# Kernel optimization log

Hardware: AMD Instinct MI355X
Metric: run time of the kernel (lower is better)

The kernel has to match this reference:

```python
import jax, jax.numpy as jnp
import numpy as np

N_NODES = 100000
NINP = 128
N_EDGES = 1600000
EPS = 1e-12


def _gcn_conv(x, W, b, src, dst, deg_inv_sqrt):
    # PyG GCNConv: h = x W; out = D^{-1/2}(A+I)D^{-1/2} h + b
    h = x @ W  # [N, out_dim]
    norm = deg_inv_sqrt[src] * deg_inv_sqrt[dst]  # [E]
    agg = jax.ops.segment_sum(h[src] * norm[:, None], dst, num_segments=N_NODES)
    # self-loop contribution: weight deg_inv_sqrt[i]^2
    agg = agg + h * (deg_inv_sqrt ** 2)[:, None]
    return agg + b


def setup_inputs() -> dict:
    key = jax.random.key(0)
    k1, k2, k3, k4 = jax.random.split(key, 4)
    edge_index = jax.random.randint(k1, (2, N_EDGES), 0, N_NODES, dtype=jnp.int64)
    # embedding table (xavier-normal-like), padding_idx=0 row zeroed
    emb = jax.random.normal(k2, (N_NODES, NINP), dtype=jnp.float32) * (2.0 / (N_NODES + NINP)) ** 0.5
    emb = emb.at[0].set(0.0)
    W1 = jax.random.normal(k3, (NINP, 2 * NINP), dtype=jnp.float32) * (1.0 / NINP) ** 0.5
    b1 = jnp.zeros((2 * NINP,), dtype=jnp.float32)
    W2 = jax.random.normal(k4, (2 * NINP, NINP), dtype=jnp.float32) * (1.0 / (2 * NINP)) ** 0.5
    b2 = jnp.zeros((NINP,), dtype=jnp.float32)
    return {"emb": emb, "W1": W1, "b1": b1, "W2": W2, "b2": b2, "edge_index": edge_index}


def reference(emb, W1, b1, W2, b2, edge_index):
    src, dst = edge_index[0], edge_index[1]
    # symmetric GCN degree with self-loops (in-degree on dst + 1)
    deg = jax.ops.segment_sum(jnp.ones_like(dst, dtype=emb.dtype), dst, num_segments=N_NODES) + 1.0
    deg_inv_sqrt = jax.lax.rsqrt(deg)
    x = _gcn_conv(emb, W1, b1, src, dst, deg_inv_sqrt)  # [N, 2*ninp]
    # F.normalize(p=2, dim=-1)
    x = x / jnp.maximum(jnp.linalg.norm(x, axis=-1, keepdims=True), EPS)
    # dropout in eval mode (identity)
    out = _gcn_conv(x, W2, b2, src, dst, deg_inv_sqrt)  # [N, ninp]
    return out
```

## Files before the change

kernel.cpp:

```cpp
#include <hip/hip_runtime.h>
#include <hip/hip_bf16.h>

typedef __attribute__((ext_vector_type(8))) short bf16x8;
typedef __attribute__((ext_vector_type(4))) float f32x4;

#define NBUCK 391
#define BCAP 8192


__device__ __forceinline__ ushort f2bf(float f) {
    unsigned int b = __float_as_uint(f);
    unsigned int r = (b + 0x7fffu + ((b >> 16) & 1u)) >> 16;
    return (ushort)r;
}
__device__ __forceinline__ float bflo(uint v) { return __uint_as_float(v << 16); }
__device__ __forceinline__ float bfhi(uint v) { return __uint_as_float(v & 0xffff0000u); }


__global__ __launch_bounds__(256) void prep_kernel(const float* __restrict__ W1, ushort* __restrict__ W1t,
                                                   const float* __restrict__ W2, ushort* __restrict__ W2t,
                                                   int* __restrict__ gcur) {
    int b = blockIdx.x, t = threadIdx.x;
    if (b == 0) {
        if (t < NBUCK) gcur[t] = 0;
        if (t + 256 < NBUCK) gcur[t + 256] = 0;
    } else if (b <= 128) {
        int i = (b - 1) * 256 + t;
        int n = i >> 7, k = i & 127;
        W1t[i] = f2bf(W1[(size_t)k * 256 + n]);
    } else {
        int i = (b - 129) * 256 + t;
        int n = i >> 8, k = i & 255;
        W2t[i] = f2bf(W2[(size_t)k * 128 + n]);
    }
}


__global__ __launch_bounds__(256) void bucket_kernel(const int* __restrict__ src, const int* __restrict__ dst,
                                                     int* __restrict__ gcur, int2* __restrict__ pairs,
                                                     int E, int chunk) {
    __shared__ int lcnt[NBUCK];
    for (int t = threadIdx.x; t < NBUCK; t += 256) lcnt[t] = 0;
    __syncthreads();
    int e0 = blockIdx.x * chunk;
    int e1 = e0 + chunk; if (e1 > E) e1 = E;
    for (int e = e0 + (int)threadIdx.x; e < e1; e += 256)
        atomicAdd(&lcnt[dst[e] >> 8], 1);
    __syncthreads();
    for (int t = threadIdx.x; t < NBUCK; t += 256) {
        int c = lcnt[t];
        lcnt[t] = c ? atomicAdd(&gcur[t], c) : 0;
    }
    __syncthreads();
    for (int e = e0 + (int)threadIdx.x; e < e1; e += 256) {
        int d = dst[e], s = src[e];
        int b = d >> 8;
        int p = atomicAdd(&lcnt[b], 1);
        if (p < BCAP) pairs[(size_t)b * BCAP + p] = make_int2(d, s);
    }
}


__global__ __launch_bounds__(512) void scan_buckets(const int* __restrict__ gcur, int* __restrict__ bbase,
                                                    int* __restrict__ offs, int Nn, int E) {
    int i = threadIdx.x;
    int v = (i < NBUCK) ? min(gcur[i], BCAP) : 0;
    int lane = i & 63, wid = i >> 6;
    int x = v;
#pragma unroll
    for (int d = 1; d < 64; d <<= 1) {
        int y = __shfl_up(x, d, 64);
        if (lane >= d) x += y;
    }
    __shared__ int wsum[8], wpre[8];
    if (lane == 63) wsum[wid] = x;
    __syncthreads();
    if (i == 0) {
        int run = 0;
        for (int w = 0; w < 8; ++w) { wpre[w] = run; run += wsum[w]; }
        offs[Nn] = E;
    }
    __syncthreads();
    if (i < NBUCK) bbase[i] = x - v + wpre[wid];
}


__global__ __launch_bounds__(256) void csr_kernel(const int2* __restrict__ pairs, const int* __restrict__ gcur,
                                                  const int* __restrict__ bbase,
                                                  int* __restrict__ offs, float* __restrict__ dis,
                                                  int* __restrict__ csr, int Nn) {
    int b = blockIdx.x;
    int n0 = b << 8;
    int ne = min(gcur[b], BCAP);
    __shared__ int cnt[256], off[256], pos[256];
    int i = threadIdx.x;
    cnt[i] = 0;
    __syncthreads();
    const int2* pp = pairs + (size_t)b * BCAP;
    for (int e = i; e < ne; e += 256)
        atomicAdd(&cnt[pp[e].x - n0], 1);
    __syncthreads();
    int lane = i & 63, wid = i >> 6;
    int v = cnt[i];
    int x = v;
#pragma unroll
    for (int d = 1; d < 64; d <<= 1) {
        int y = __shfl_up(x, d, 64);
        if (lane >= d) x += y;
    }
    __shared__ int wsum[4], wpre[4];
    if (lane == 63) wsum[wid] = x;
    __syncthreads();
    if (i == 0) {
        int run = 0;
        for (int w = 0; w < 4; ++w) { wpre[w] = run; run += wsum[w]; }
    }
    __syncthreads();
    int excl = x - v + wpre[wid];
    off[i] = excl;
    pos[i] = 0;
    int n = n0 + i;
    if (n < Nn) {
        offs[n] = bbase[b] + excl;
        dis[n] = rsqrtf((float)v + 1.0f);
    }
    __syncthreads();
    int base = bbase[b];
    for (int e = i; e < ne; e += 256) {
        int2 r = pp[e];
        int li = r.x - n0;
        int p = atomicAdd(&pos[li], 1);
        csr[base + off[li] + p] = r.y;
    }
}


__global__ void cast_scale_kernel(const float4* __restrict__ in, const float* __restrict__ dis,
                                  ushort4* __restrict__ out, int n4) {
    int stride = gridDim.x * blockDim.x;
    for (int i = blockIdx.x * blockDim.x + threadIdx.x; i < n4; i += stride) {
        float s = dis[i >> 5];
        float4 v = in[i];
        ushort4 o;
        o.x = f2bf(v.x * s); o.y = f2bf(v.y * s); o.z = f2bf(v.z * s); o.w = f2bf(v.w * s);
        out[i] = o;
    }
}


template <bool BIAS, bool BF16OUT>
__global__ __launch_bounds__(256) void agg_kernel(const uint* __restrict__ tbl,
                                                  const int* __restrict__ offs,
                                                  const int* __restrict__ rec,
                                                  const float* __restrict__ dis,
                                                  const float* __restrict__ bias,
                                                  void* __restrict__ outp, int Nn) {
    int gw = (int)((blockIdx.x * 256 + threadIdx.x) >> 6);
    uint lane = threadIdx.x & 63;
    if (gw >= Nn) return;
    float dn = dis[gw];
    int e0 = offs[gw], e1 = offs[gw + 1];
    uint hv = tbl[(uint)gw * 64u + lane];
    float ax = bflo(hv), ay = bfhi(hv);

    for (int base = e0; base < e1; base += 16) {
        int ee = base + (int)(lane & 15u);
        uint rr = (uint)rec[ee < e1 ? ee : e1 - 1];
        uint vv[16];
#pragma unroll
        for (int j = 0; j < 16; ++j) {
            uint idx = (uint)__shfl((int)rr, j, 64);
            vv[j] = tbl[idx * 64u + lane];
        }
#pragma unroll
        for (int j = 0; j < 16; ++j) {
            uint v = (base + j < e1) ? vv[j] : 0u;
            ax += bflo(v);
            ay += bfhi(v);
        }
    }

    ax *= dn; ay *= dn;
    if (BIAS) {
        float2 bv = reinterpret_cast<const float2*>(bias)[lane];
        ax += bv.x; ay += bv.y;
    }
    if (BF16OUT) {
        reinterpret_cast<uint*>(outp)[(uint)gw * 64u + lane] =
            (uint)f2bf(ax) | ((uint)f2bf(ay) << 16);
    } else {
        float2 o; o.x = ax; o.y = ay;
        reinterpret_cast<float2*>(outp)[(uint)gw * 64u + lane] = o;
    }
}


__global__ __launch_bounds__(256, 2) void fused_gemm(const ushort* __restrict__ A,
                                                     const ushort* __restrict__ W1t,
                                                     const float* __restrict__ bias1,
                                                     const ushort* __restrict__ W2t,
                                                     const float* __restrict__ dsc,
                                                     ushort* __restrict__ out2, int M) {
    __shared__ ushort xt[64 * 256];
    __shared__ float ssl[4][64];
    int lane = threadIdx.x & 63, wid = threadIdx.x >> 6;
    int m0 = blockIdx.x * 64;
    int koff = (lane >> 4) * 8;

    bf16x8 a[4][4], b1f[4][4];
#pragma unroll
    for (int ms = 0; ms < 4; ++ms) {
        int r = m0 + ms * 16 + (lane & 15);
        if (r >= M) r = M - 1;
        const bf16x8* p = reinterpret_cast<const bf16x8*>(A + (size_t)r * 128 + koff);
#pragma unroll
        for (int ks = 0; ks < 4; ++ks) a[ms][ks] = p[ks * 4];
    }
#pragma unroll
    for (int ns = 0; ns < 4; ++ns) {
        int c = wid * 64 + ns * 16 + (lane & 15);
        const bf16x8* p = reinterpret_cast<const bf16x8*>(W1t + (size_t)c * 128 + koff);
#pragma unroll
        for (int ks = 0; ks < 4; ++ks) b1f[ns][ks] = p[ks * 4];
    }

    f32x4 acc[4][4];
#pragma unroll
    for (int ms = 0; ms < 4; ++ms)
#pragma unroll
        for (int ns = 0; ns < 4; ++ns) acc[ms][ns] = (f32x4){0.f, 0.f, 0.f, 0.f};
#pragma unroll
    for (int ks = 0; ks < 4; ++ks)
#pragma unroll
        for (int ms = 0; ms < 4; ++ms)
#pragma unroll
            for (int ns = 0; ns < 4; ++ns)
                acc[ms][ns] = __builtin_amdgcn_mfma_f32_16x16x32_bf16(a[ms][ks], b1f[ns][ks], acc[ms][ns], 0, 0, 0);

    bf16x8 b2f[2][8];
#pragma unroll
    for (int ns = 0; ns < 2; ++ns) {
        int c = wid * 32 + ns * 16 + (lane & 15);
        const bf16x8* p = reinterpret_cast<const bf16x8*>(W2t + (size_t)c * 256 + koff);
#pragma unroll
        for (int ks = 0; ks < 8; ++ks) b2f[ns][ks] = p[ks * 4];
    }

    float bv[4];
#pragma unroll
    for (int ns = 0; ns < 4; ++ns) bv[ns] = bias1[wid * 64 + ns * 16 + (lane & 15)];
    float ps[4][4];
#pragma unroll
    for (int ms = 0; ms < 4; ++ms)
#pragma unroll
        for (int r = 0; r < 4; ++r) {
            float s = 0.f;
#pragma unroll
            for (int ns = 0; ns < 4; ++ns) {
                float v = acc[ms][ns][r] + bv[ns];
                acc[ms][ns][r] = v;
                s += v * v;
            }
            ps[ms][r] = s;
        }
#pragma unroll
    for (int d = 1; d < 16; d <<= 1)
#pragma unroll
        for (int ms = 0; ms < 4; ++ms)
#pragma unroll
            for (int r = 0; r < 4; ++r) ps[ms][r] += __shfl_xor(ps[ms][r], d, 64);
    if ((lane & 15) == 0) {
#pragma unroll
        for (int ms = 0; ms < 4; ++ms)
#pragma unroll
            for (int r = 0; r < 4; ++r) ssl[wid][ms * 16 + (lane >> 4) * 4 + r] = ps[ms][r];
    }
    __syncthreads();
#pragma unroll
    for (int ms = 0; ms < 4; ++ms)
#pragma unroll
        for (int r = 0; r < 4; ++r) {
            int rt = ms * 16 + (lane >> 4) * 4 + r;
            float tot = ssl[0][rt] + ssl[1][rt] + ssl[2][rt] + ssl[3][rt];
            float inv = 1.0f / fmaxf(sqrtf(tot), 1e-12f);
            int sw = (rt & 7) << 3;
#pragma unroll
            for (int ns = 0; ns < 4; ++ns) {
                int col = wid * 64 + ns * 16 + (lane & 15);
                xt[(rt * 256 + col) ^ sw] = f2bf(acc[ms][ns][r] * inv);
            }
        }
    __syncthreads();

    f32x4 acc2[4][2];
#pragma unroll
    for (int ms = 0; ms < 4; ++ms)
#pragma unroll
        for (int ns = 0; ns < 2; ++ns) acc2[ms][ns] = (f32x4){0.f, 0.f, 0.f, 0.f};
#pragma unroll
    for (int ks = 0; ks < 8; ++ks) {
        bf16x8 a2[4];
#pragma unroll
        for (int ms = 0; ms < 4; ++ms) {
            int rowA = ms * 16 + (lane & 15);
            int eb = (rowA * 256 + koff + ks * 32) ^ ((rowA & 7) << 3);
            a2[ms] = *reinterpret_cast<const bf16x8*>(&xt[eb]);
        }
#pragma unroll
        for (int ms = 0; ms < 4; ++ms)
#pragma unroll
            for (int ns = 0; ns < 2; ++ns)
                acc2[ms][ns] = __builtin_amdgcn_mfma_f32_16x16x32_bf16(a2[ms], b2f[ns][ks], acc2[ms][ns], 0, 0, 0);
    }
#pragma unroll
    for (int ms = 0; ms < 4; ++ms)
#pragma unroll
        for (int r = 0; r < 4; ++r) {
            int row = m0 + ms * 16 + (lane >> 4) * 4 + r;
            if (row < M) {
                float sc = dsc[row];
#pragma unroll
                for (int ns = 0; ns < 2; ++ns)
                    out2[(size_t)row * 128 + wid * 32 + ns * 16 + (lane & 15)] =
                        f2bf(acc2[ms][ns][r] * sc);
            }
        }
}


extern "C" void kernel_launch(void* const* d_in, const int* in_sizes, int n_in,
                              void* d_out, int out_size, void* d_ws, size_t ws_size,
                              hipStream_t stream) {
    const float* emb = (const float*)d_in[0];
    const float* W1 = (const float*)d_in[1];
    const float* b1 = (const float*)d_in[2];
    const float* W2 = (const float*)d_in[3];
    const float* b2 = (const float*)d_in[4];
    const int* eidx = (const int*)d_in[5];

    const int Nn = in_sizes[0] / 128;
    const int E = in_sizes[5] / 2;
    const int* srcp = eidx;
    const int* dstp = eidx + E;

    float* ws = (float*)d_ws;
    size_t o = 0;
    uint* tbl1 = (uint*)(ws + o);  o += (size_t)Nn * 64;
    uint* axb = (uint*)(ws + o);   o += (size_t)Nn * 64;
    uint* tbl2 = (uint*)(ws + o);  o += (size_t)Nn * 64;
    ushort* W1t = (ushort*)(ws + o); o += 128 * 256 / 2;
    ushort* W2t = (ushort*)(ws + o); o += 256 * 128 / 2;
    float* dis = ws + o;    o += Nn;
    int* gcur = (int*)(ws + o);   o += NBUCK + 1;
    int* bbase = (int*)(ws + o);  o += NBUCK + 1;
    int* offs = (int*)(ws + o);   o += Nn + 16;
    int* csr = (int*)(ws + o);    o += E;
    int2* pairs = (int2*)(ws + o); o += (size_t)NBUCK * BCAP * 2;

    prep_kernel<<<257, 256, 0, stream>>>(W1, W1t, W2, W2t, gcur);

    int B1B = 512;
    int chunk = (E + B1B - 1) / B1B;
    bucket_kernel<<<B1B, 256, 0, stream>>>(srcp, dstp, gcur, pairs, E, chunk);
    scan_buckets<<<1, 512, 0, stream>>>(gcur, bbase, offs, Nn, E);
    csr_kernel<<<NBUCK, 256, 0, stream>>>(pairs, gcur, bbase, offs, dis, csr, Nn);

    int n4 = Nn * 128 / 4;
    cast_scale_kernel<<<2048, 256, 0, stream>>>((const float4*)emb, dis, (ushort4*)tbl1, n4);

    agg_kernel<false, true><<<(Nn + 3) / 4, 256, 0, stream>>>(tbl1, offs, csr, dis, nullptr, axb, Nn);
    fused_gemm<<<(Nn + 63) / 64, 256, 0, stream>>>((const ushort*)axb, W1t, b1, W2t, dis, (ushort*)tbl2, Nn);

    agg_kernel<true, false><<<(Nn + 3) / 4, 256, 0, stream>>>(tbl2, offs, csr, dis, b2, d_out, Nn);
}
```

Before: 244.2 us.

## Give each wavefront whole rows in fused GEMM to drop block-level syncs

The fused two-layer GEMM kernel is restructured so each wavefront owns 16 complete rows across all 256 hidden columns, rather than a 64-column slice of 64 rows shared by the block. The row L2-norm is then reduced with intra-wave shuffles alone, and the normalized tile goes into a per-wave LDS region, which removes both __syncthreads and the cross-wave partial-sum array. The cost is that every wave now loads the full W1 and W2 weight fragments from global/L2 inside the k-loops instead of holding a per-wave slice in registers, so weight traffic per wave rises and register pressure shifts.

New measurement: 294.2 us. 1.2x slower.

```diff
diff --git a/kernel.cpp b/kernel.cpp
--- a/kernel.cpp
+++ b/kernel.cpp
@@ -201,130 +201,93 @@
                                                      const ushort* __restrict__ W2t,
                                                      const float* __restrict__ dsc,
                                                      ushort* __restrict__ out2, int M) {
-    __shared__ ushort xt[64 * 256];
-    __shared__ float ssl[4][64];
+    __shared__ __align__(16) char xls[4 * 8192];
     int lane = threadIdx.x & 63, wid = threadIdx.x >> 6;
-    int m0 = blockIdx.x * 64;
-    int koff = (lane >> 4) * 8;
-
-    bf16x8 a[4][4], b1f[4][4];
-#pragma unroll
-    for (int ms = 0; ms < 4; ++ms) {
-        int r = m0 + ms * 16 + (lane & 15);
-        if (r >= M) r = M - 1;
-        const bf16x8* p = reinterpret_cast<const bf16x8*>(A + (size_t)r * 128 + koff);
-#pragma unroll
-        for (int ks = 0; ks < 4; ++ks) a[ms][ks] = p[ks * 4];
-    }
-#pragma unroll
-    for (int ns = 0; ns < 4; ++ns) {
-        int c = wid * 64 + ns * 16 + (lane & 15);
-        const bf16x8* p = reinterpret_cast<const bf16x8*>(W1t + (size_t)c * 128 + koff);
-#pragma unroll
-        for (int ks = 0; ks < 4; ++ks) b1f[ns][ks] = p[ks * 4];
-    }
-
-    f32x4 acc[4][4];
-#pragma unroll
-    for (int ms = 0; ms < 4; ++ms)
-#pragma unroll
-        for (int ns = 0; ns < 4; ++ns) acc[ms][ns] = (f32x4){0.f, 0.f, 0.f, 0.f};
-#pragma unroll
-    for (int ks = 0; ks < 4; ++ks)
-#pragma unroll
-        for (int ms = 0; ms < 4; ++ms)
-#pragma unroll
-            for (int ns = 0; ns < 4; ++ns)
-                acc[ms][ns] = __builtin_amdgcn_mfma_f32_16x16x32_bf16(a[ms][ks], b1f[ns][ks], acc[ms][ns], 0, 0, 0);
-
-    bf16x8 b2f[2][8];
-#pragma unroll
-    for (int ns = 0; ns < 2; ++ns) {
-        int c = wid * 32 + ns * 16 + (lane & 15);
-        const bf16x8* p = reinterpret_cast<const bf16x8*>(W2t + (size_t)c * 256 + koff);
-#pragma unroll
-        for (int ks = 0; ks < 8; ++ks) b2f[ns][ks] = p[ks * 4];
-    }
-
-    float bv[4];
-#pragma unroll
-    for (int ns = 0; ns < 4; ++ns) bv[ns] = bias1[wid * 64 + ns * 16 + (lane & 15)];
-    float ps[4][4];
-#pragma unroll
-    for (int ms = 0; ms < 4; ++ms)
-#pragma unroll
-        for (int r = 0; r < 4; ++r) {
-            float s = 0.f;
-#pragma unroll
-            for (int ns = 0; ns < 4; ++ns) {
-                float v = acc[ms][ns][r] + bv[ns];
-                acc[ms][ns][r] = v;
-                s += v * v;
-            }
-            ps[ms][r] = s;
-        }
+    int g = lane >> 4;
+    int i15 = lane & 15;
+    int koff = g * 8;
+    int r0 = blockIdx.x * 64 + wid * 16;
+    char* lds = xls + wid * 8192;
+
+    int arow = r0 + i15; if (arow >= M) arow = M - 1;
+    const bf16x8* ap = reinterpret_cast<const bf16x8*>(A + (size_t)arow * 128 + koff);
+    bf16x8 af[4];
+#pragma unroll
+    for (int ks = 0; ks < 4; ++ks) af[ks] = ap[ks * 4];
+
+    f32x4 acc[16];
+#pragma unroll
+    for (int ns = 0; ns < 16; ++ns) acc[ns] = (f32x4){0.f, 0.f, 0.f, 0.f};
+
+#pragma unroll
+    for (int ks = 0; ks < 4; ++ks) {
+        bf16x8 bf_[16];
+#pragma unroll
+        for (int ns = 0; ns < 16; ++ns)
+            bf_[ns] = *reinterpret_cast<const bf16x8*>(W1t + (size_t)(ns * 16 + i15) * 128 + ks * 32 + koff);
+#pragma unroll
+        for (int ns = 0; ns < 16; ++ns)
+            acc[ns] = __builtin_amdgcn_mfma_f32_16x16x32_bf16(af[ks], bf_[ns], acc[ns], 0, 0, 0);
+    }
+
+    float ps[4];
+#pragma unroll
+    for (int r = 0; r < 4; ++r) {
+        float s = 0.f;
+#pragma unroll
+        for (int ns = 0; ns < 16; ++ns) {
+            float v = acc[ns][r] + bias1[ns * 16 + i15];
+            acc[ns][r] = v;
+            s += v * v;
+        }
+        ps[r] = s;
+    }
 #pragma unroll
     for (int d = 1; d < 16; d <<= 1)
 #pragma unroll
-        for (int ms = 0; ms < 4; ++ms)
-#pragma unroll
-            for (int r = 0; r < 4; ++r) ps[ms][r] += __shfl_xor(ps[ms][r], d, 64);
-    if ((lane & 15) == 0) {
-#pragma unroll
-        for (int ms = 0; ms < 4; ++ms)
-#pragma unroll
-            for (int r = 0; r < 4; ++r) ssl[wid][ms * 16 + (lane >> 4) * 4 + r] = ps[ms][r];
-    }
-    __syncthreads();
-#pragma unroll
-    for (int ms = 0; ms < 4; ++ms)
-#pragma unroll
-        for (int r = 0; r < 4; ++r) {
-            int rt = ms * 16 + (lane >> 4) * 4 + r;
-            float tot = ssl[0][rt] + ssl[1][rt] + ssl[2][rt] + ssl[3][rt];
-            float inv = 1.0f / fmaxf(sqrtf(tot), 1e-12f);
-            int sw = (rt & 7) << 3;
-#pragma unroll
-            for (int ns = 0; ns < 4; ++ns) {
-                int col = wid * 64 + ns * 16 + (lane & 15);
-                xt[(rt * 256 + col) ^ sw] = f2bf(acc[ms][ns][r] * inv);
-            }
-        }
-    __syncthreads();
-
-    f32x4 acc2[4][2];
-#pragma unroll
-    for (int ms = 0; ms < 4; ++ms)
-#pragma unroll
-        for (int ns = 0; ns < 2; ++ns) acc2[ms][ns] = (f32x4){0.f, 0.f, 0.f, 0.f};
+        for (int r = 0; r < 4; ++r) ps[r] += __shfl_xor(ps[r], d, 64);
+    float inv[4];
+#pragma unroll
+    for (int r = 0; r < 4; ++r) inv[r] = 1.0f / fmaxf(sqrtf(ps[r]), 1e-12f);
+
+#pragma unroll
+    for (int r = 0; r < 4; ++r) {
+        int rt = g * 4 + r;
+        int sw = (rt & 7) << 4;
+#pragma unroll
+        for (int ns = 0; ns < 16; ++ns) {
+            int byte = rt * 512 + (ns * 16 + i15) * 2;
+            *reinterpret_cast<ushort*>(lds + (byte ^ sw)) = f2bf(acc[ns][r] * inv[r]);
+        }
+    }
+
+    f32x4 acc2[8];
+#pragma unroll
+    for (int ns = 0; ns < 8; ++ns) acc2[ns] = (f32x4){0.f, 0.f, 0.f, 0.f};
+    int sw2 = (i15 & 7) << 4;
 #pragma unroll
     for (int ks = 0; ks < 8; ++ks) {
-        bf16x8 a2[4];
-#pragma unroll
-        for (int ms = 0; ms < 4; ++ms) {
-            int rowA = ms * 16 + (lane & 15);
-            int eb = (rowA * 256 + koff + ks * 32) ^ ((rowA & 7) << 3);
-            a2[ms] = *reinterpret_cast<const bf16x8*>(&xt[eb]);
-        }
-#pragma unroll
-        for (int ms = 0; ms < 4; ++ms)
-#pragma unroll
-            for (int ns = 0; ns < 2; ++ns)
-                acc2[ms][ns] = __builtin_amdgcn_mfma_f32_16x16x32_bf16(a2[ms], b2f[ns][ks], acc2[ms][ns], 0, 0, 0);
-    }
-#pragma unroll
-    for (int ms = 0; ms < 4; ++ms)
-#pragma unroll
-        for (int r = 0; r < 4; ++r) {
-            int row = m0 + ms * 16 + (lane >> 4) * 4 + r;
-            if (row < M) {
-                float sc = dsc[row];
-#pragma unroll
-                for (int ns = 0; ns < 2; ++ns)
-                    out2[(size_t)row * 128 + wid * 32 + ns * 16 + (lane & 15)] =
-                        f2bf(acc2[ms][ns][r] * sc);
-            }
-        }
+        int rbyte = i15 * 512 + ks * 64 + g * 16;
+        bf16x8 a2 = *reinterpret_cast<const bf16x8*>(lds + (rbyte ^ sw2));
+        bf16x8 b2[8];
+#pragma unroll
+        for (int ns = 0; ns < 8; ++ns)
+            b2[ns] = *reinterpret_cast<const bf16x8*>(W2t + (size_t)(ns * 16 + i15) * 256 + ks * 32 + koff);
+#pragma unroll
+        for (int ns = 0; ns < 8; ++ns)
+            acc2[ns] = __builtin_amdgcn_mfma_f32_16x16x32_bf16(a2, b2[ns], acc2[ns], 0, 0, 0);
+    }
+
+#pragma unroll
+    for (int r = 0; r < 4; ++r) {
+        int row = r0 + g * 4 + r;
+        if (row < M) {
+            float sc = dsc[row];
+#pragma unroll
+            for (int ns = 0; ns < 8; ++ns)
+                out2[(size_t)row * 128 + ns * 16 + i15] = f2bf(acc2[ns][r] * sc);
+        }
+    }
 }
 
 
```

## Fuse first-layer aggregation into the fused GEMM kernel via shared memory

Applied to the files above, without the earlier changes.

The first-layer neighbor aggregation is moved into the fused GEMM kernel. Each wave gathers and sums bf16 neighbor rows for 16 nodes and writes the aggregated tile into swizzled shared memory, which the MFMA GEMM then reads. This removes one kernel launch and the global write and re-read of the intermediate aggregated buffer. In exchange, gather latency now runs inside a kernel limited to about 2 blocks per CU by its shared-memory and register use, so occupancy for the irregular gathers may be lower than in the standalone aggregation kernel.

After: 283.2 us. +16.0%, slower.

```diff
diff --git a/kernel.cpp b/kernel.cpp
--- a/kernel.cpp
+++ b/kernel.cpp
@@ -195,30 +195,69 @@
 }
 
 
-__global__ __launch_bounds__(256, 2) void fused_gemm(const ushort* __restrict__ A,
-                                                     const ushort* __restrict__ W1t,
-                                                     const float* __restrict__ bias1,
-                                                     const ushort* __restrict__ W2t,
-                                                     const float* __restrict__ dsc,
-                                                     ushort* __restrict__ out2, int M) {
-    __shared__ ushort xt[64 * 256];
+__global__ __launch_bounds__(256, 2) void fused_all(const uint* __restrict__ tbl,
+                                                    const int* __restrict__ offs,
+                                                    const int* __restrict__ rec,
+                                                    const float* __restrict__ dis,
+                                                    const ushort* __restrict__ W1t,
+                                                    const float* __restrict__ bias1,
+                                                    const ushort* __restrict__ W2t,
+                                                    ushort* __restrict__ out2, int M) {
+    __shared__ __align__(16) char xls[64 * 256 * 2];
     __shared__ float ssl[4][64];
     int lane = threadIdx.x & 63, wid = threadIdx.x >> 6;
+    int g = lane >> 4;
+    int i15 = lane & 15;
+    int koff = g * 8;
     int m0 = blockIdx.x * 64;
-    int koff = (lane >> 4) * 8;
+
+    for (int t = 0; t < 16; ++t) {
+        int local = wid * 16 + t;
+        int gw = m0 + local;
+        uint res = 0;
+        if (gw < M) {
+            float dn = dis[gw];
+            int e0 = offs[gw], e1 = offs[gw + 1];
+            uint hv = tbl[(uint)gw * 64u + lane];
+            float ax = bflo(hv), ay = bfhi(hv);
+            for (int base = e0; base < e1; base += 16) {
+                int ee = base + i15;
+                uint rr = (uint)rec[ee < e1 ? ee : e1 - 1];
+                uint vv[16];
+#pragma unroll
+                for (int j = 0; j < 16; ++j) {
+                    uint idx = (uint)__shfl((int)rr, j, 64);
+                    vv[j] = tbl[idx * 64u + lane];
+                }
+#pragma unroll
+                for (int j = 0; j < 16; ++j) {
+                    uint v = (base + j < e1) ? vv[j] : 0u;
+                    ax += bflo(v);
+                    ay += bfhi(v);
+                }
+            }
+            ax *= dn; ay *= dn;
+            res = (uint)f2bf(ax) | ((uint)f2bf(ay) << 16);
+        }
+        int byte = local * 256 + (int)lane * 4;
+        *reinterpret_cast<uint*>(xls + (byte ^ ((local & 7) << 4))) = res;
+    }
+    __syncthreads();
 
     bf16x8 a[4][4], b1f[4][4];
 #pragma unroll
     for (int ms = 0; ms < 4; ++ms) {
-        int r = m0 + ms * 16 + (lane & 15);
-        if (r >= M) r = M - 1;
-        const bf16x8* p = reinterpret_cast<const bf16x8*>(A + (size_t)r * 128 + koff);
-#pragma unroll
-        for (int ks = 0; ks < 4; ++ks) a[ms][ks] = p[ks * 4];
+        int row = ms * 16 + i15;
+        int sw = (row & 7) << 4;
+#pragma unroll
+        for (int ks = 0; ks < 4; ++ks) {
+            int byte = row * 256 + g * 16 + ks * 64;
+            a[ms][ks] = *reinterpret_cast<const bf16x8*>(xls + (byte ^ sw));
+        }
     }
 #pragma unroll
     for (int ns = 0; ns < 4; ++ns) {
-        int c = wid * 64 + ns * 16 + (lane & 15);
+        int c = wid * 64 + ns * 16 + i15;
         const bf16x8* p = reinterpret_cast<const bf16x8*>(W1t + (size_t)c * 128 + koff);
 #pragma unroll
         for (int ks = 0; ks < 4; ++ks) b1f[ns][ks] = p[ks * 4];
@@ -240,7 +279,7 @@
     bf16x8 b2f[2][8];
 #pragma unroll
     for (int ns = 0; ns < 2; ++ns) {
-        int c = wid * 32 + ns * 16 + (lane & 15);
+        int c = wid * 32 + ns * 16 + i15;
         const bf16x8* p = reinterpret_cast<const bf16x8*>(W2t + (size_t)c * 256 + koff);
 #pragma unroll
         for (int ks = 0; ks < 8; ++ks) b2f[ns][ks] = p[ks * 4];
@@ -248,7 +287,7 @@
 
     float bv[4];
 #pragma unroll
-    for (int ns = 0; ns < 4; ++ns) bv[ns] = bias1[wid * 64 + ns * 16 + (lane & 15)];
+    for (int ns = 0; ns < 4; ++ns) bv[ns] = bias1[wid * 64 + ns * 16 + i15];
     float ps[4][4];
 #pragma unroll
     for (int ms = 0; ms < 4; ++ms)
@@ -269,24 +308,26 @@
         for (int ms = 0; ms < 4; ++ms)
 #pragma unroll
             for (int r = 0; r < 4; ++r) ps[ms][r] += __shfl_xor(ps[ms][r], d, 64);
-    if ((lane & 15) == 0) {
+    if (i15 == 0) {
 #pragma unroll
         for (int ms = 0; ms < 4; ++ms)
 #pragma unroll
-            for (int r = 0; r < 4; ++r) ssl[wid][ms * 16 + (lane >> 4) * 4 + r] = ps[ms][r];
-    }
-    __syncthreads();
+            for (int r = 0; r < 4; ++r) ssl[wid][ms * 16 + g * 4 + r] = ps[ms][r];
+    }
+    __syncthreads();
+
+    ushort* xt = reinterpret_cast<ushort*>(xls);
 #pragma unroll
     for (int ms = 0; ms < 4; ++ms)
 #pragma unroll
         for (int r = 0; r < 4; ++r) {
-            int rt = ms * 16 + (lane >> 4) * 4 + r;
+            int rt = ms * 16 + g * 4 + r;
             float tot = ssl[0][rt] + ssl[1][rt] + ssl[2][rt] + ssl[3][rt];
             float inv = 1.0f / fmaxf(sqrtf(tot), 1e-12f);
             int sw = (rt & 7) << 3;
 #pragma unroll
             for (int ns = 0; ns < 4; ++ns) {
-                int col = wid * 64 + ns * 16 + (lane & 15);
+                int col = wid * 64 + ns * 16 + i15;
                 xt[(rt * 256 + col) ^ sw] = f2bf(acc[ms][ns][r] * inv);
             }
         }
@@ -302,7 +343,7 @@
         bf16x8 a2[4];
 #pragma unroll
         for (int ms = 0; ms < 4; ++ms) {
-            int rowA = ms * 16 + (lane & 15);
+            int rowA = ms * 16 + i15;
             int eb = (rowA * 256 + koff + ks * 32) ^ ((rowA & 7) << 3);
             a2[ms] = *reinterpret_cast<const bf16x8*>(&xt[eb]);
         }
@@ -316,13 +357,12 @@
     for (int ms = 0; ms < 4; ++ms)
 #pragma unroll
         for (int r = 0; r < 4; ++r) {
-            int row = m0 + ms * 16 + (lane >> 4) * 4 + r;
+            int row = m0 + ms * 16 + g * 4 + r;
             if (row < M) {
-                float sc = dsc[row];
+                float sc = dis[row];
 #pragma unroll
                 for (int ns = 0; ns < 2; ++ns)
-                    out2[(size_t)row * 128 + wid * 32 + ns * 16 + (lane & 15)] =
-                        f2bf(acc2[ms][ns][r] * sc);
+                    out2[(size_t)row * 128 + wid * 32 + ns * 16 + i15] = f2bf(acc2[ms][ns][r] * sc);
             }
         }
 }
@@ -346,7 +386,6 @@
     float* ws = (float*)d_ws;
     size_t o = 0;
     uint* tbl1 = (uint*)(ws + o);  o += (size_t)Nn * 64;
-    uint* axb = (uint*)(ws + o);   o += (size_t)Nn * 64;
     uint* tbl2 = (uint*)(ws + o);  o += (size_t)Nn * 64;
     ushort* W1t = (ushort*)(ws + o); o += 128 * 256 / 2;
     ushort* W2t = (ushort*)(ws + o); o += 256 * 128 / 2;
@@ -368,8 +407,7 @@
     int n4 = Nn * 128 / 4;
     cast_scale_kernel<<<2048, 256, 0, stream>>>((const float4*)emb, dis, (ushort4*)tbl1, n4);
 
-    agg_kernel<false, true><<<(Nn + 3) / 4, 256, 0, stream>>>(tbl1, offs, csr, dis, nullptr, axb, Nn);
-    fused_gemm<<<(Nn + 63) / 64, 256, 0, stream>>>((const ushort*)axb, W1t, b1, W2t, dis, (ushort*)tbl2, Nn);
+    fused_all<<<(Nn + 63) / 64, 256, 0, stream>>>(tbl1, offs, csr, dis, W1t, b1, W2t, (ushort*)tbl2, Nn);
 
     agg_kernel<true, false><<<(Nn + 3) / 4, 256, 0, stream>>>(tbl2, offs, csr, dis, b2, d_out, Nn);
 }
```
